# Optimization experiments

Measured on AMD Instinct MI355X. Metric: run time of the kernel, lower is better.

Reference implementation:

```python
import jax, jax.numpy as jnp
import numpy as np

NEG_INF = -1.0e9
LN_EPS = 1e-5
LEAK = 0.2


def setup_inputs() -> dict:
    key = jax.random.key(0)
    ks = jax.random.split(key, 8)
    B, C, T, N, H = 8, 64, 24, 512, 2
    hd = C // H
    x = jax.random.normal(ks[0], (B, C, T, N), dtype=jnp.float32)
    gso = jax.random.randint(ks[1], (N, N), 0, 2, dtype=jnp.int32)
    # torch nn.Linear weights are (out, in); xavier-ish scale
    s = (2.0 / (C + C)) ** 0.5
    Wq = jax.random.normal(ks[2], (C, C), dtype=jnp.float32) * s
    Wk = jax.random.normal(ks[3], (C, C), dtype=jnp.float32) * s
    Wv = jax.random.normal(ks[4], (C, C), dtype=jnp.float32) * s
    sa = (2.0 / (H + hd)) ** 0.5
    a_src = jax.random.normal(ks[5], (H, hd), dtype=jnp.float32) * sa
    a_dst = jax.random.normal(ks[6], (H, hd), dtype=jnp.float32) * sa
    ln_gamma = jnp.ones((C,), dtype=jnp.float32)
    ln_beta = jnp.zeros((C,), dtype=jnp.float32)
    return {"x": x, "gso": gso, "Wq": Wq, "Wk": Wk, "Wv": Wv,
            "a_src": a_src, "a_dst": a_dst, "ln_gamma": ln_gamma, "ln_beta": ln_beta}


def _spatial_gat(x, gso, Wq, Wk, Wv, a_src, a_dst, ln_gamma, ln_beta):
    B, C, T, N = x.shape
    H, hd = a_src.shape
    # (B, C, T, N) -> (B*T, N, C)
    xr = jnp.transpose(x, (0, 2, 3, 1)).reshape(B * T, N, C)
    # torch Linear: y = x @ W.T
    Q = jnp.einsum('bnc,dc->bnd', xr, Wq).reshape(B * T, N, H, hd)
    K = jnp.einsum('bnc,dc->bnd', xr, Wk).reshape(B * T, N, H, hd)
    V = jnp.einsum('bnc,dc->bnd', xr, Wv).reshape(B * T, N, H, hd)
    # additive GAT scores, all heads at once
    s_src = jnp.einsum('bnhd,hd->bnh', Q, a_src)  # (BT, N, H)
    s_dst = jnp.einsum('bnhd,hd->bnh', K, a_dst)  # (BT, N, H)
    scores = jax.nn.leaky_relu(s_src[:, :, None, :] + s_dst[:, None, :, :], LEAK)  # (BT, Ni, Nj, H)
    mask = jnp.where(gso == 0, jnp.float32(NEG_INF), jnp.float32(0.0))  # (N, N)
    scores = scores + mask[None, :, :, None]
    attn = jax.nn.softmax(scores, axis=2)  # softmax over destination j
    out = jnp.einsum('bijh,bjhd->bihd', attn, V)  # (BT, N, H, hd)
    out = out.reshape(B * T, N, C)
    # LayerNorm over channel dim
    mu = jnp.mean(out, axis=-1, keepdims=True)
    var = jnp.var(out, axis=-1, keepdims=True)
    out = (out - mu) * jax.lax.rsqrt(var + LN_EPS) * ln_gamma + ln_beta
    # back to (B, C, T, N)
    return jnp.transpose(out.reshape(B, T, N, C), (0, 3, 1, 2))


def reference(x, gso, Wq, Wk, Wv, a_src, a_dst, ln_gamma, ln_beta):
    return _spatial_gat(x, gso, Wq, Wk, Wv, a_src, a_dst, ln_gamma, ln_beta)
```

## Files before the change

kernel.cpp:

```cpp
#include <hip/hip_runtime.h>

#define CDIM 64
#define TDIM 24
#define NDIM 512
#define NBT  192

typedef float    float4v __attribute__((ext_vector_type(4)));
typedef _Float16 half8v  __attribute__((ext_vector_type(8)));
typedef _Float16 half4v  __attribute__((ext_vector_type(4)));
typedef _Float16 half2v  __attribute__((ext_vector_type(2)));


__device__ __forceinline__ float exp2_fast(float x) {
#if __has_builtin(__builtin_amdgcn_exp2f)
  return __builtin_amdgcn_exp2f(x);
#else
  return __expf(x * 0.69314718f);
#endif
}

struct SmemK1 {
  union {
    _Float16 xt[128][72];
    _Float16 vtb[64][136];
  } big;
  _Float16 wv[64][72];
  _Float16 wext[16][72];
};

__launch_bounds__(256, 4)
__global__ void k1_v(const float* __restrict__ x,  const float* __restrict__ Wv,
                     const float* __restrict__ Wq, const float* __restrict__ Wk,
                     const float* __restrict__ a_src, const float* __restrict__ a_dst,
                     const int* __restrict__ gso,
                     _Float16* __restrict__ VT_g,
                     float* __restrict__ s_src_g, float* __restrict__ s_dst_g,
                     unsigned char* __restrict__ maskb) {
  const int t  = threadIdx.x;
  const int bx = blockIdx.x;

  if (bx >= 768) {
    int g = (bx - 768) * 256 + t;
    const int4* gp = (const int4*)gso + (size_t)g * 4;
    unsigned w[4];
#pragma unroll
    for (int k = 0; k < 4; ++k) {
      int4 v = gp[k];
      w[k] = (v.x ? 0x000000FFu : 0u) | (v.y ? 0x0000FF00u : 0u) |
             (v.z ? 0x00FF0000u : 0u) | (v.w ? 0xFF000000u : 0u);
    }
    uint4 o; o.x = w[0]; o.y = w[1]; o.z = w[2]; o.w = w[3];
    ((uint4*)maskb)[g] = o;
    return;
  }

  __shared__ SmemK1 sm;
  const int qn = bx & 3;
  const int bt = bx >> 2;
  const int b  = bt / TDIM, tt = bt % TDIM;
  const int n0 = qn * 128;

  for (int it = 0; it < 16; ++it) {
    int idx = it * 256 + t;
    sm.wv[idx >> 6][idx & 63] = (_Float16)Wv[idx];
  }
  for (int z = t; z < 12 * 72; z += 256) ((_Float16*)sm.wext[4])[z] = (_Float16)0.f;
  if (t < 64) {
    int c = t;
    float s0 = 0.f, s1 = 0.f, d0 = 0.f, d1 = 0.f;
#pragma unroll
    for (int d = 0; d < 32; ++d) {
      s0 += a_src[d]      * Wq[d * 64 + c];
      s1 += a_src[32 + d] * Wq[(32 + d) * 64 + c];
      d0 += a_dst[d]      * Wk[d * 64 + c];
      d1 += a_dst[32 + d] * Wk[(32 + d) * 64 + c];
    }
    const float l2e = 1.44269504f;
    sm.wext[0][c] = (_Float16)(s0 * l2e); sm.wext[1][c] = (_Float16)(s1 * l2e);
    sm.wext[2][c] = (_Float16)(d0 * l2e); sm.wext[3][c] = (_Float16)(d1 * l2e);
  }
  for (int it = 0; it < 16; ++it) {
    int idx = it * 256 + t;
    int cp = idx >> 7, n = idx & 127;
    int c0 = cp * 2;
    const float* base = x + ((size_t)(b * CDIM + c0) * TDIM + tt) * NDIM + n0 + n;
    half2v p; p[0] = (_Float16)base[0]; p[1] = (_Float16)base[(size_t)TDIM * NDIM];
    *(half2v*)&sm.big.xt[n][c0] = p;
  }
  __syncthreads();

  const int lane = t & 63, w = t >> 6;
  const int m = lane & 15, quad = lane >> 4;
  const int mbase = w * 32;

  float4v acc[2][5];
#pragma unroll
  for (int mt = 0; mt < 2; ++mt)
#pragma unroll
    for (int nt = 0; nt < 5; ++nt)
#pragma unroll
      for (int r = 0; r < 4; ++r) acc[mt][nt][r] = 0.f;

#pragma unroll
  for (int ks = 0; ks < 2; ++ks) {
    half8v af[2], bf[5];
#pragma unroll
    for (int mt = 0; mt < 2; ++mt)
      af[mt] = *(const half8v*)&sm.big.xt[mbase + mt * 16 + m][ks * 32 + quad * 8];
#pragma unroll
    for (int nt = 0; nt < 4; ++nt)
      bf[nt] = *(const half8v*)&sm.wv[nt * 16 + m][ks * 32 + quad * 8];
    bf[4] = *(const half8v*)&sm.wext[m][ks * 32 + quad * 8];
#pragma unroll
    for (int mt = 0; mt < 2; ++mt)
#pragma unroll
      for (int nt = 0; nt < 5; ++nt)
        acc[mt][nt] = __builtin_amdgcn_mfma_f32_16x16x32_f16(af[mt], bf[nt], acc[mt][nt], 0, 0, 0);
  }

  if (m < 4) {
    float* basep = (m < 2 ? s_src_g : s_dst_g) + (size_t)(bt * 2 + (m & 1)) * NDIM;
#pragma unroll
    for (int mt = 0; mt < 2; ++mt)
#pragma unroll
      for (int r = 0; r < 4; ++r)
        basep[n0 + mbase + mt * 16 + quad * 4 + r] = acc[mt][4][r];
  }
  __syncthreads();

#pragma unroll
  for (int mt = 0; mt < 2; ++mt)
#pragma unroll
    for (int nt = 0; nt < 4; ++nt)
#pragma unroll
      for (int r = 0; r < 4; r += 2) {
        int nl = mbase + mt * 16 + quad * 4 + r;
        int c  = nt * 16 + m;
        half2v p = __builtin_bit_cast(half2v,
            __builtin_amdgcn_cvt_pkrtz(acc[mt][nt][r], acc[mt][nt][r + 1]));
        *(half2v*)&sm.big.vtb[c][nl] = p;
      }
  __syncthreads();

  const unsigned* vdw = (const unsigned*)sm.big.vtb;
  unsigned* outdw = (unsigned*)VT_g;
  for (int it = 0; it < 16; ++it) {
    int idx = it * 256 + t;
    int c = idx >> 6, jd = idx & 63;
    outdw[(size_t)(bt * 64 + c) * 256 + qn * 64 + jd] = vdw[c * 68 + jd];
  }
}

struct SmemK2 {
  union {
    struct { _Float16 vt[64][128]; unsigned char mb[64][144]; } s;
    struct { float otile[64][66]; float rsum[4][64]; float rsq[4][64];
             float mu[64]; float rs[64]; } e;
  } u;
  _Float16 sF16[2][512];
  _Float16 sP16[2][512];
};

__launch_bounds__(256, 4)
__global__ void k2_attn(const _Float16* __restrict__ VT_g,
                        const float* __restrict__ s_src_g, const float* __restrict__ s_dst_g,
                        const unsigned char* __restrict__ maskb,
                        const float* __restrict__ gamma, const float* __restrict__ beta,
                        float* __restrict__ out) {
  __shared__ SmemK2 sm;
  const int t     = threadIdx.x;
  const int id    = blockIdx.x;
  const int itile = (id >> 3) & 7;
  const int bt    = ((id >> 6) << 3) | (id & 7);
  const int i0    = itile * 64;
  const int b     = bt / TDIM, tt = bt % TDIM;
  const int lane  = t & 63, w = t >> 6;
  const int h = w >> 1, ihalf = w & 1;
  const int m = lane & 15, quad = lane >> 4;

  for (int it = 0; it < 4; ++it) {
    int idx = it * 256 + t;
    float d = s_dst_g[(size_t)bt * 2 * NDIM + idx];
    ((_Float16*)sm.sF16)[idx] = (_Float16)exp2_fast(d);
    ((_Float16*)sm.sP16)[idx] = (_Float16)exp2_fast(0.2f * d);
  }
  half8v E8[2], Q8[2];
#pragma unroll
  for (int mt = 0; mt < 2; ++mt) {
    float sv = s_src_g[(size_t)(bt * 2 + h) * NDIM + i0 + ihalf * 32 + mt * 16 + m];
    _Float16 ev = (_Float16)exp2_fast(sv - 6.f);
    _Float16 qv = (_Float16)exp2_fast(0.2f * sv - 6.f);
#pragma unroll
    for (int jj = 0; jj < 8; ++jj) { E8[mt][jj] = ev; Q8[mt][jj] = qv; }
  }

  float4v acc[2][2], accs[2];
#pragma unroll
  for (int mt = 0; mt < 2; ++mt) {
#pragma unroll
    for (int r = 0; r < 4; ++r) { acc[mt][0][r] = 0.f; acc[mt][1][r] = 0.f; accs[mt][r] = 0.f; }
  }
  const half8v bones = {(_Float16)1.f, (_Float16)1.f, (_Float16)1.f, (_Float16)1.f,
                        (_Float16)1.f, (_Float16)1.f, (_Float16)1.f, (_Float16)1.f};

  const uint4* vsrc = (const uint4*)VT_g;
  uint4 pv0, pv1, pv2, pv3, pm0, pm1;
  const int vc  = t >> 4;
  const int vch = t & 15;
  const int mc  = t >> 3;
  const int mch = t & 7;
  const int vswz = (vch * 8) ^ ((vc & 7) * 8);

#define PREFETCH(js_)                                                          \
  {                                                                            \
    pv0 = vsrc[(size_t)(bt * 64 + vc     ) * 64 + (js_) * 16 + vch];           \
    pv1 = vsrc[(size_t)(bt * 64 + vc + 16) * 64 + (js_) * 16 + vch];           \
    pv2 = vsrc[(size_t)(bt * 64 + vc + 32) * 64 + (js_) * 16 + vch];           \
    pv3 = vsrc[(size_t)(bt * 64 + vc + 48) * 64 + (js_) * 16 + vch];           \
    pm0 = *(const uint4*)(maskb + (size_t)(i0 + mc     ) * NDIM +              \
                          (js_) * 128 + mch * 16);                             \
    pm1 = *(const uint4*)(maskb + (size_t)(i0 + mc + 32) * NDIM +              \
                          (js_) * 128 + mch * 16);                             \
  }

  PREFETCH(0);

  for (int js = 0; js < 4; ++js) {
    __syncthreads();
    *(uint4*)&sm.u.s.vt[vc     ][vswz] = pv0;
    *(uint4*)&sm.u.s.vt[vc + 16][vswz] = pv1;
    *(uint4*)&sm.u.s.vt[vc + 32][vswz] = pv2;
    *(uint4*)&sm.u.s.vt[vc + 48][vswz] = pv3;
    *(uint4*)&sm.u.s.mb[mc     ][mch * 16] = pm0;
    *(uint4*)&sm.u.s.mb[mc + 32][mch * 16] = pm1;
    __syncthreads();
    if (js < 3) PREFETCH(js + 1);

#pragma unroll
    for (int ksl = 0; ksl < 4; ++ksl) {
      int jq = ksl * 32 + quad * 8;
      half8v F8 = *(const half8v*)&sm.sF16[h][js * 128 + jq];
      half8v P8 = *(const half8v*)&sm.sP16[h][js * 128 + jq];
      int vbase = (h * 32 + m) * 128 + (jq ^ ((m & 7) * 8));
      half8v b0 = *(const half8v*)&sm.u.s.vt[0][vbase];
      half8v b1 = *(const half8v*)&sm.u.s.vt[0][vbase + 16 * 128];
#pragma unroll
      for (int mt = 0; mt < 2; ++mt) {
        const unsigned* mwp = (const unsigned*)&sm.u.s.mb[ihalf * 32 + mt * 16 + m][jq];
        unsigned mw0 = mwp[0], mw1 = mwp[1];
        half8v e8 = __builtin_elementwise_max(E8[mt] * F8, Q8[mt] * P8);
        uint4 eu = __builtin_bit_cast(uint4, e8);
        eu.x &= __builtin_amdgcn_perm(0u, mw0, 0x01010000u);
        eu.y &= __builtin_amdgcn_perm(0u, mw0, 0x03030202u);
        eu.z &= __builtin_amdgcn_perm(0u, mw1, 0x01010000u);
        eu.w &= __builtin_amdgcn_perm(0u, mw1, 0x03030202u);
        half8v af = __builtin_bit_cast(half8v, eu);
        acc[mt][0] = __builtin_amdgcn_mfma_f32_16x16x32_f16(af, b0,    acc[mt][0], 0, 0, 0);
        acc[mt][1] = __builtin_amdgcn_mfma_f32_16x16x32_f16(af, b1,    acc[mt][1], 0, 0, 0);
        accs[mt]   = __builtin_amdgcn_mfma_f32_16x16x32_f16(af, bones, accs[mt],   0, 0, 0);
      }
    }
  }
#undef PREFETCH

  __syncthreads();
#pragma unroll
  for (int mt = 0; mt < 2; ++mt)
#pragma unroll
    for (int r = 0; r < 4; ++r) {
      float sc = __builtin_amdgcn_rcpf(accs[mt][r]);
      int i_loc = ihalf * 32 + mt * 16 + quad * 4 + r;
#pragma unroll
      for (int nt = 0; nt < 2; ++nt)
        sm.u.e.otile[i_loc][h * 32 + nt * 16 + m] = acc[mt][nt][r] * sc;
    }
  __syncthreads();

  {
    int i = t & 63, cg = t >> 6;
    float s1 = 0.f, s2 = 0.f;
#pragma unroll
    for (int cc = 0; cc < 16; ++cc) {
      float v = sm.u.e.otile[i][cg * 16 + cc];
      s1 += v; s2 += v * v;
    }
    sm.u.e.rsum[cg][i] = s1;
    sm.u.e.rsq[cg][i]  = s2;
  }
  __syncthreads();
  if (t < 64) {
    int i = t;
    float s1 = 0.f, s2 = 0.f;
#pragma unroll
    for (int cg = 0; cg < 4; ++cg) { s1 += sm.u.e.rsum[cg][i]; s2 += sm.u.e.rsq[cg][i]; }
    float mu  = s1 * (1.f / 64.f);
    float var = s2 * (1.f / 64.f) - mu * mu;
    sm.u.e.mu[i] = mu;
    sm.u.e.rs[i] = rsqrtf(var + 1e-5f);
  }
  __syncthreads();
  {
    int i = t & 63, cg = t >> 6;
    float mu = sm.u.e.mu[i], rs = sm.u.e.rs[i];
    int n = i0 + i;
#pragma unroll
    for (int cc = 0; cc < 16; ++cc) {
      int c = cg * 16 + cc;
      float v = (sm.u.e.otile[i][c] - mu) * rs * gamma[c] + beta[c];
      out[((size_t)(b * CDIM + c) * TDIM + tt) * NDIM + n] = v;
    }
  }
}

extern "C" void kernel_launch(void* const* d_in, const int* in_sizes, int n_in,
                              void* d_out, int out_size, void* d_ws, size_t ws_size,
                              hipStream_t stream) {
  const float* x     = (const float*)d_in[0];
  const int*   gso   = (const int*)d_in[1];
  const float* Wq    = (const float*)d_in[2];
  const float* Wk    = (const float*)d_in[3];
  const float* Wv    = (const float*)d_in[4];
  const float* a_src = (const float*)d_in[5];
  const float* a_dst = (const float*)d_in[6];
  const float* gamma = (const float*)d_in[7];
  const float* beta  = (const float*)d_in[8];
  float* out = (float*)d_out;

  char* ws = (char*)d_ws;
  _Float16* VT_g  = (_Float16*)ws;
  float*    s_src = (float*)(ws + 12582912);
  float*    s_dst = (float*)(ws + 13369344);
  unsigned char* maskb = (unsigned char*)(ws + 14155776);

  k1_v<<<832, 256, 0, stream>>>(x, Wv, Wq, Wk, a_src, a_dst, gso,
                                VT_g, s_src, s_dst, maskb);
  k2_attn<<<1536, 256, 0, stream>>>(VT_g, s_src, s_dst, maskb, gamma, beta, out);
}
```

Measured before the change: 122.9 us.

## Load mask directly into registers, vectorize V weight and output copies

In the attention kernel, the mask is no longer staged through shared memory. Each lane reads its own mask bytes straight from global memory into registers for every j-slice, which drops the shared mask array and its stores. The k1 kernel now converts Wv with float4 loads and writes VT with uint4 stores instead of scalar dwords, and its launch bound is relaxed to 2 blocks per SM. The mask loads are now issued per slice with no prefetch and are less coalesced, so latency may be exposed, while the relaxed bound may reduce occupancy.

Result: slower. 127.4 us (+3.6%).

```diff
diff --git a/kernel.cpp b/kernel.cpp
--- a/kernel.cpp
+++ b/kernel.cpp
@@ -28,7 +28,7 @@
   _Float16 wext[16][72];
 };
 
-__launch_bounds__(256, 4)
+__launch_bounds__(256, 2)
 __global__ void k1_v(const float* __restrict__ x,  const float* __restrict__ Wv,
                      const float* __restrict__ Wq, const float* __restrict__ Wk,
                      const float* __restrict__ a_src, const float* __restrict__ a_dst,
@@ -60,9 +60,14 @@
   const int b  = bt / TDIM, tt = bt % TDIM;
   const int n0 = qn * 128;
 
-  for (int it = 0; it < 16; ++it) {
+#pragma unroll
+  for (int it = 0; it < 4; ++it) {
     int idx = it * 256 + t;
-    sm.wv[idx >> 6][idx & 63] = (_Float16)Wv[idx];
+    float4 vv = ((const float4*)Wv)[idx];
+    int d = idx >> 4, k4 = (idx & 15) * 4;
+    half4v h4; h4[0] = (_Float16)vv.x; h4[1] = (_Float16)vv.y;
+    h4[2] = (_Float16)vv.z; h4[3] = (_Float16)vv.w;
+    *(half4v*)&sm.wv[d][k4] = h4;
   }
   for (int z = t; z < 12 * 72; z += 256) ((_Float16*)sm.wext[4])[z] = (_Float16)0.f;
   if (t < 64) {
@@ -142,18 +147,18 @@
       }
   __syncthreads();
 
-  const unsigned* vdw = (const unsigned*)sm.big.vtb;
-  unsigned* outdw = (unsigned*)VT_g;
-  for (int it = 0; it < 16; ++it) {
+  const uint4* vq = (const uint4*)sm.big.vtb;
+#pragma unroll
+  for (int it = 0; it < 4; ++it) {
     int idx = it * 256 + t;
-    int c = idx >> 6, jd = idx & 63;
-    outdw[(size_t)(bt * 64 + c) * 256 + qn * 64 + jd] = vdw[c * 68 + jd];
+    int c = idx >> 4, q4 = idx & 15;
+    ((uint4*)VT_g)[(size_t)(bt * 64 + c) * 64 + qn * 16 + q4] = vq[c * 17 + q4];
   }
 }
 
 struct SmemK2 {
   union {
-    struct { _Float16 vt[64][128]; unsigned char mb[64][144]; } s;
+    struct { _Float16 vt[64][128]; } s;
     struct { float otile[64][66]; float rsum[4][64]; float rsq[4][64];
              float mu[64]; float rs[64]; } e;
   } u;
@@ -204,12 +209,13 @@
                         (_Float16)1.f, (_Float16)1.f, (_Float16)1.f, (_Float16)1.f};
 
   const uint4* vsrc = (const uint4*)VT_g;
-  uint4 pv0, pv1, pv2, pv3, pm0, pm1;
+  uint4 pv0, pv1, pv2, pv3;
   const int vc  = t >> 4;
   const int vch = t & 15;
-  const int mc  = t >> 3;
-  const int mch = t & 7;
   const int vswz = (vch * 8) ^ ((vc & 7) * 8);
+
+  const unsigned char* mb0 = maskb + (size_t)(i0 + ihalf * 32 + m) * NDIM + quad * 8;
+  const unsigned char* mb1 = mb0 + (size_t)16 * NDIM;
 
 #define PREFETCH(js_)                                                          \
   {                                                                            \
@@ -217,24 +223,28 @@
     pv1 = vsrc[(size_t)(bt * 64 + vc + 16) * 64 + (js_) * 16 + vch];           \
     pv2 = vsrc[(size_t)(bt * 64 + vc + 32) * 64 + (js_) * 16 + vch];           \
     pv3 = vsrc[(size_t)(bt * 64 + vc + 48) * 64 + (js_) * 16 + vch];           \
-    pm0 = *(const uint4*)(maskb + (size_t)(i0 + mc     ) * NDIM +              \
-                          (js_) * 128 + mch * 16);                             \
-    pm1 = *(const uint4*)(maskb + (size_t)(i0 + mc + 32) * NDIM +              \
-                          (js_) * 128 + mch * 16);                             \
   }
 
   PREFETCH(0);
 
+#pragma unroll
   for (int js = 0; js < 4; ++js) {
     __syncthreads();
     *(uint4*)&sm.u.s.vt[vc     ][vswz] = pv0;
     *(uint4*)&sm.u.s.vt[vc + 16][vswz] = pv1;
     *(uint4*)&sm.u.s.vt[vc + 32][vswz] = pv2;
     *(uint4*)&sm.u.s.vt[vc + 48][vswz] = pv3;
-    *(uint4*)&sm.u.s.mb[mc     ][mch * 16] = pm0;
-    *(uint4*)&sm.u.s.mb[mc + 32][mch * 16] = pm1;
     __syncthreads();
     if (js < 3) PREFETCH(js + 1);
+
+    uint2 mk[2][4];
+#pragma unroll
+    for (int mt = 0; mt < 2; ++mt) {
+      const unsigned char* mbp = (mt ? mb1 : mb0) + js * 128;
+#pragma unroll
+      for (int ksl = 0; ksl < 4; ++ksl)
+        mk[mt][ksl] = *(const uint2*)(mbp + ksl * 32);
+    }
 
 #pragma unroll
     for (int ksl = 0; ksl < 4; ++ksl) {
@@ -246,8 +256,7 @@
       half8v b1 = *(const half8v*)&sm.u.s.vt[0][vbase + 16 * 128];
 #pragma unroll
       for (int mt = 0; mt < 2; ++mt) {
-        const unsigned* mwp = (const unsigned*)&sm.u.s.mb[ihalf * 32 + mt * 16 + m][jq];
-        unsigned mw0 = mwp[0], mw1 = mwp[1];
+        unsigned mw0 = mk[mt][ksl].x, mw1 = mk[mt][ksl].y;
         half8v e8 = __builtin_elementwise_max(E8[mt] * F8, Q8[mt] * P8);
         uint4 eu = __builtin_bit_cast(uint4, e8);
         eu.x &= __builtin_amdgcn_perm(0u, mw0, 0x01010000u);
```
